# Kernel optimization log

Measured on AMD Instinct MI355X. Metric: run time of the kernel, lower is better.

## Reference

```python
import jax, jax.numpy as jnp
import numpy as np

N = 50000        # nodes
E = 800000       # edges (before self-loops)
F_IN = 128       # input node features
HID = 64         # GAT hidden per head
HEADS1 = 4
NUM_GRAPHS = 64
NEG_SLOPE = 0.2  # PyG GATConv default leaky_relu slope


def setup_inputs() -> dict:
    key = jax.random.key(0)
    ks = jax.random.split(key, 12)
    x = jax.random.normal(ks[0], (N, F_IN), dtype=jnp.float32)
    edge_index = jax.random.randint(ks[1], (2, E), 0, N, dtype=jnp.int32)
    batch = jnp.sort(jax.random.randint(ks[2], (N,), 0, NUM_GRAPHS, dtype=jnp.int32))
    s = 1.0 / np.sqrt(F_IN)
    W1 = jax.random.uniform(ks[3], (F_IN, HEADS1 * HID), jnp.float32, -s, s)
    att_src1 = jax.random.uniform(ks[4], (HEADS1, HID), jnp.float32, -s, s)
    att_dst1 = jax.random.uniform(ks[5], (HEADS1, HID), jnp.float32, -s, s)
    b1 = jnp.zeros((HEADS1 * HID,), jnp.float32)
    s2 = 1.0 / np.sqrt(HEADS1 * HID)
    W2 = jax.random.uniform(ks[6], (HEADS1 * HID, HID), jnp.float32, -s2, s2)
    att_src2 = jax.random.uniform(ks[7], (1, HID), jnp.float32, -s2, s2)
    att_dst2 = jax.random.uniform(ks[8], (1, HID), jnp.float32, -s2, s2)
    b2 = jnp.zeros((HID,), jnp.float32)
    return {"x": x, "edge_index": edge_index, "batch": batch,
            "W1": W1, "att_src1": att_src1, "att_dst1": att_dst1, "b1": b1,
            "W2": W2, "att_src2": att_src2, "att_dst2": att_dst2, "b2": b2}


def gat_conv(x, src, dst, W, a_src, a_dst, bias, heads, out_dim):
    # PyG GATConv: h = x @ W (no lin bias); per-node attention logits;
    # e_ij = leaky_relu(alpha_src[j] + alpha_dst[i]); softmax over dst groups;
    # out_i = sum_j alpha_ij * h_j; concat heads; + bias.
    n = x.shape[0]
    h = (x @ W).reshape(n, heads, out_dim)                 # [N,H,C]
    alpha_src = jnp.einsum('nhc,hc->nh', h, a_src)         # [N,H]
    alpha_dst = jnp.einsum('nhc,hc->nh', h, a_dst)         # [N,H]
    e = jax.nn.leaky_relu(alpha_src[src] + alpha_dst[dst], NEG_SLOPE)  # [E,H]
    m = jax.ops.segment_max(e, dst, num_segments=n)        # segment softmax (stable)
    e = jnp.exp(e - m[dst])
    denom = jax.ops.segment_sum(e, dst, num_segments=n)
    alpha = e / denom[dst]                                 # [E,H]
    msg = h[src] * alpha[:, :, None]                       # [E,H,C]
    agg = jax.ops.segment_sum(msg, dst, num_segments=n)    # [N,H,C]
    return agg.reshape(n, heads * out_dim) + bias


def reference(x, edge_index, batch, W1, att_src1, att_dst1, b1, W2, att_src2, att_dst2, b2):
    # add self loops (PyG GATConv default add_self_loops=True)
    loops = jnp.arange(N, dtype=edge_index.dtype)
    src = jnp.concatenate([edge_index[0], loops])
    dst = jnp.concatenate([edge_index[1], loops])
    h = jax.nn.relu(gat_conv(x, src, dst, W1, att_src1, att_dst1, b1, HEADS1, HID))
    h = gat_conv(h, src, dst, W2, att_src2, att_dst2, b2, 1, HID)
    # global mean pool over graphs
    sums = jax.ops.segment_sum(h, batch, num_segments=NUM_GRAPHS)
    cnt = jax.ops.segment_sum(jnp.ones((N,), h.dtype), batch, num_segments=NUM_GRAPHS)
    return sums / jnp.maximum(cnt, 1.0)[:, None]
```

## Files before the change

kernel.cpp:

```cpp
#include <hip/hip_runtime.h>
#include <math.h>


typedef unsigned short ushort_t;
typedef __bf16 bf16x8 __attribute__((ext_vector_type(8)));
typedef float  f32x4  __attribute__((ext_vector_type(4)));

__device__ inline float bf2f(ushort_t u) { return __uint_as_float((unsigned)u << 16); }
__device__ inline ushort_t f2bf(float x) {
  unsigned b = __float_as_uint(x);
  return (ushort_t)((b + 0x7fff + ((b >> 16) & 1)) >> 16);
}
__device__ inline float leaky(float v) { return (v > 0.f) ? v : 0.2f * v; }

__device__ inline f32x4 mfma16(bf16x8 a, bf16x8 b, f32x4 c) {
  return __builtin_amdgcn_mfma_f32_16x16x32_bf16(a, b, c, 0, 0, 0);
}

__global__ void k_zero_i32(int* __restrict__ p, int n) {
  int i = blockIdx.x * blockDim.x + threadIdx.x;
  if (i < n) p[i] = 0;
}

__global__ void k_hist(const int* __restrict__ edst, int E, int N, int* __restrict__ deg) {
  int stride = gridDim.x * blockDim.x;
  int EE = E + N;
  for (int i = blockIdx.x * blockDim.x + threadIdx.x; i < EE; i += stride) {
    int d = (i < E) ? edst[i] : (i - E);
    atomicAdd(&deg[d], 1);
  }
}

__global__ void k_gbounds(const int* __restrict__ batch, int N, int G,
                          int* __restrict__ gstart) {
  int stride = gridDim.x * blockDim.x;
  for (int i = blockIdx.x * blockDim.x + threadIdx.x; i < N; i += stride) {
    int b = batch[i];
    int bp = (i == 0) ? -1 : batch[i - 1];
    for (int g = bp + 1; g <= b; ++g) gstart[g] = i;
    if (i == N - 1)
      for (int g = b + 1; g <= G; ++g) gstart[g] = N;
  }
}

__global__ void k_scan_bsum(const int* __restrict__ deg, int n, int* __restrict__ bsum) {
  __shared__ int ws[16];
  int tid = threadIdx.x, lane = tid & 63, wv = tid >> 6;
  int i = blockIdx.x * 1024 + tid;
  int v = (i < n) ? deg[i] : 0;
  #pragma unroll
  for (int off = 1; off < 64; off <<= 1) v += __shfl_xor(v, off);
  if (lane == 0) ws[wv] = v;
  __syncthreads();
  if (tid < 16) {
    int s = ws[tid];
    #pragma unroll
    for (int off = 1; off < 16; off <<= 1) s += __shfl_xor(s, off);
    if (tid == 0) bsum[blockIdx.x] = s;
  }
}

__global__ void k_scan_bbase(const int* __restrict__ bsum, int nb,
                             int* __restrict__ bbase, int* __restrict__ offsets, int n) {
  int lane = threadIdx.x & 63;
  int v = (lane < nb) ? bsum[lane] : 0;
  int x = v;
  #pragma unroll
  for (int off = 1; off < 64; off <<= 1) {
    int t = __shfl_up(x, off);
    if (lane >= off) x += t;
  }
  if (lane < nb) bbase[lane] = x - v;
  if (lane == nb - 1) offsets[n] = x;
}

__global__ void k_scan_final(const int* __restrict__ deg, int n,
                             const int* __restrict__ bbase,
                             int* __restrict__ offsets, int* __restrict__ cursor) {
  __shared__ int wsum[16];
  int tid = threadIdx.x, lane = tid & 63, wv = tid >> 6;
  int i = blockIdx.x * 1024 + tid;
  int v = (i < n) ? deg[i] : 0;
  int x = v;
  #pragma unroll
  for (int off = 1; off < 64; off <<= 1) {
    int t = __shfl_up(x, off);
    if (lane >= off) x += t;
  }
  if (lane == 63) wsum[wv] = x;
  __syncthreads();
  if (wv == 0 && lane < 16) {
    int s = wsum[lane];
    #pragma unroll
    for (int off = 1; off < 16; off <<= 1) {
      int t = __shfl_up(s, off);
      if (lane >= off) s += t;
    }
    wsum[lane] = s;
  }
  __syncthreads();
  int wbase = (wv == 0) ? 0 : wsum[wv - 1];
  int incl = bbase[blockIdx.x] + wbase + x;
  if (i < n) { int o = incl - v; offsets[i] = o; cursor[i] = o; }
}

__global__ void k_scatter(const int* __restrict__ esrc, const int* __restrict__ edst,
                          int E, int N, int* __restrict__ cursor,
                          int* __restrict__ ssrc, int* __restrict__ sdst) {
  int stride = gridDim.x * blockDim.x;
  int EE = E + N;
  for (int i = blockIdx.x * blockDim.x + threadIdx.x; i < EE; i += stride) {
    int d, s;
    if (i < E) { d = edst[i]; s = esrc[i]; }
    else       { d = i - E;   s = i - E;   }
    int pos = atomicAdd(&cursor[d], 1);
    ssrc[pos] = s;
    sdst[pos] = d;
  }
}


__global__ void k_packA_f32(const float* __restrict__ A, ushort_t* __restrict__ ah,
                            ushort_t* __restrict__ al, int M, int K, int MF) {
  int KT = K >> 5;
  int total = MF * KT * 64;
  int t = blockIdx.x * blockDim.x + threadIdx.x;
  if (t >= total) return;
  int l = t & 63, fa = t >> 6;
  int mt = fa / KT, kt = fa - mt * KT;
  int row = mt * 16 + (l & 15);
  int k0 = kt * 32 + (l >> 4) * 8;
  float v[8];
  if (row < M) {
    float4 v0 = *(const float4*)(A + (size_t)row * K + k0);
    float4 v1 = *(const float4*)(A + (size_t)row * K + k0 + 4);
    v[0] = v0.x; v[1] = v0.y; v[2] = v0.z; v[3] = v0.w;
    v[4] = v1.x; v[5] = v1.y; v[6] = v1.z; v[7] = v1.w;
  } else {
    #pragma unroll
    for (int j = 0; j < 8; ++j) v[j] = 0.f;
  }
  ushort_t h[8], lo[8];
  #pragma unroll
  for (int j = 0; j < 8; ++j) {
    h[j] = f2bf(v[j]);
    lo[j] = f2bf(v[j] - bf2f(h[j]));
  }
  size_t o = (size_t)t * 8;
  *(ushort4*)(ah + o)     = make_ushort4(h[0], h[1], h[2], h[3]);
  *(ushort4*)(ah + o + 4) = make_ushort4(h[4], h[5], h[6], h[7]);
  *(ushort4*)(al + o)     = make_ushort4(lo[0], lo[1], lo[2], lo[3]);
  *(ushort4*)(al + o + 4) = make_ushort4(lo[4], lo[5], lo[6], lo[7]);
}

__global__ void k_packB_f32(const float* __restrict__ B, ushort_t* __restrict__ bh,
                            ushort_t* __restrict__ bl, int K, int Nn) {
  int KT = K >> 5;
  int total = (Nn >> 4) * KT * 64;
  int t = blockIdx.x * blockDim.x + threadIdx.x;
  if (t >= total) return;
  int l = t & 63, fb = t >> 6;
  int nt = fb / KT, kt = fb - nt * KT;
  int col = nt * 16 + (l & 15);
  int k0 = kt * 32 + (l >> 4) * 8;
  ushort_t h[8], lo[8];
  #pragma unroll
  for (int j = 0; j < 8; ++j) {
    float v = B[(size_t)(k0 + j) * Nn + col];
    h[j] = f2bf(v);
    lo[j] = f2bf(v - bf2f(h[j]));
  }
  size_t o = (size_t)t * 8;
  *(ushort4*)(bh + o)     = make_ushort4(h[0], h[1], h[2], h[3]);
  *(ushort4*)(bh + o + 4) = make_ushort4(h[4], h[5], h[6], h[7]);
  *(ushort4*)(bl + o)     = make_ushort4(lo[0], lo[1], lo[2], lo[3]);
  *(ushort4*)(bl + o + 4) = make_ushort4(lo[4], lo[5], lo[6], lo[7]);
}

template<int KT, int TERMS, int WM>
__global__ __launch_bounds__(256)
void k_gemm_att(const ushort_t* __restrict__ Ah, const ushort_t* __restrict__ Al,
                const ushort_t* __restrict__ Bh, const ushort_t* __restrict__ Bl,
                const float* __restrict__ a_srcW, const float* __restrict__ a_dstW,
                ushort_t* __restrict__ hb, float* __restrict__ as_,
                float* __restrict__ ad_, int M, int Nn, int H) {
  constexpr int WN = 4 / WM;
  const int tid = threadIdx.x;
  const int w = tid >> 6, lane = tid & 63;
  const int wm = w & (WM - 1), wn = w / WM;
  const int m0w = blockIdx.x * (WM * 32) + wm * 32;
  const int n0  = blockIdx.y * (WN * 64) + wn * 64;
  const int head = n0 >> 6;
  const int mt0 = m0w >> 4, nt0 = n0 >> 4;

  const ushort_t* pAh[2];
  const ushort_t* pAl[2];
  const ushort_t* pBh[4];
  const ushort_t* pBl[4];
  #pragma unroll
  for (int mi = 0; mi < 2; ++mi) {
    size_t fa = (size_t)(mt0 + mi) * KT;
    pAh[mi] = Ah + fa * 512 + (size_t)lane * 8;
    if constexpr (TERMS == 3) pAl[mi] = Al + fa * 512 + (size_t)lane * 8;
  }
  #pragma unroll
  for (int ni = 0; ni < 4; ++ni) {
    size_t fb = (size_t)(nt0 + ni) * KT;
    pBh[ni] = Bh + fb * 512 + (size_t)lane * 8;
    pBl[ni] = Bl + fb * 512 + (size_t)lane * 8;
  }

  f32x4 acc[2][4];
  #pragma unroll
  for (int mi = 0; mi < 2; ++mi)
    #pragma unroll
    for (int ni = 0; ni < 4; ++ni)
      acc[mi][ni] = (f32x4){0.f, 0.f, 0.f, 0.f};

  for (int kt = 0; kt < KT; ++kt) {
    const size_t ko = (size_t)kt * 512;
    bf16x8 ahf[2], alf[2], bhf[4], blf[4];
    #pragma unroll
    for (int mi = 0; mi < 2; ++mi) {
      ahf[mi] = *(const bf16x8*)(pAh[mi] + ko);
      if constexpr (TERMS == 3) alf[mi] = *(const bf16x8*)(pAl[mi] + ko);
    }
    #pragma unroll
    for (int ni = 0; ni < 4; ++ni) {
      bhf[ni] = *(const bf16x8*)(pBh[ni] + ko);
      blf[ni] = *(const bf16x8*)(pBl[ni] + ko);
    }
    #pragma unroll
    for (int mi = 0; mi < 2; ++mi)
      #pragma unroll
      for (int ni = 0; ni < 4; ++ni) {
        if constexpr (TERMS == 3)
          acc[mi][ni] = mfma16(alf[mi], bhf[ni], acc[mi][ni]);
        acc[mi][ni] = mfma16(ahf[mi], blf[ni], acc[mi][ni]);
        acc[mi][ni] = mfma16(ahf[mi], bhf[ni], acc[mi][ni]);
      }
  }

  const int c16 = lane & 15, q = lane >> 4;
  float sv[4], dv[4];
  #pragma unroll
  for (int ni = 0; ni < 4; ++ni) {
    sv[ni] = a_srcW[head * 64 + ni * 16 + c16];
    dv[ni] = a_dstW[head * 64 + ni * 16 + c16];
  }
  #pragma unroll
  for (int mi = 0; mi < 2; ++mi) {
    #pragma unroll
    for (int r = 0; r < 4; ++r) {
      int gr = m0w + mi * 16 + q * 4 + r;
      float ps = acc[mi][0][r] * sv[0] + acc[mi][1][r] * sv[1] +
                 acc[mi][2][r] * sv[2] + acc[mi][3][r] * sv[3];
      float pd = acc[mi][0][r] * dv[0] + acc[mi][1][r] * dv[1] +
                 acc[mi][2][r] * dv[2] + acc[mi][3][r] * dv[3];
      #pragma unroll
      for (int off = 1; off < 16; off <<= 1) {
        ps += __shfl_xor(ps, off);
        pd += __shfl_xor(pd, off);
      }
      if (gr < M) {
        #pragma unroll
        for (int ni = 0; ni < 4; ++ni)
          hb[(size_t)gr * Nn + n0 + ni * 16 + c16] = f2bf(acc[mi][ni][r]);
        if (c16 == 0) { as_[gr * H + head] = ps; ad_[gr * H + head] = pd; }
      }
    }
  }
}

__global__ void k_edgew1(const int* __restrict__ ssrc, const int* __restrict__ sdst,
                         const float* __restrict__ as1, const float* __restrict__ ad1,
                         float* __restrict__ w1, int EE) {
  int t = blockIdx.x * blockDim.x + threadIdx.x;
  if (t >= EE * 4) return;
  int e = t >> 2, h = t & 3;
  int s = ssrc[e], d = sdst[e];
  w1[t] = __expf(leaky(as1[s * 4 + h] + ad1[d * 4 + h]));
}

__global__ void k_edgew2(const int* __restrict__ ssrc, const int* __restrict__ sdst,
                         const float* __restrict__ as2, const float* __restrict__ ad2,
                         float* __restrict__ w2, int EE) {
  int e = blockIdx.x * blockDim.x + threadIdx.x;
  if (e >= EE) return;
  w2[e] = __expf(leaky(as2[ssrc[e]] + ad2[sdst[e]]));
}

__global__ void k_agg1(const ushort_t* __restrict__ h1b, const float* __restrict__ w1,
                       const int* __restrict__ offs, const int* __restrict__ ssrc,
                       const float* __restrict__ b1, ushort_t* __restrict__ a2h, int N) {
  int gt = blockIdx.x * blockDim.x + threadIdx.x;
  int wid = gt >> 6, lane = gt & 63;
  if (wid >= N) return;
  int head = lane >> 4, sub = lane & 15, coff = sub << 2;
  int start = offs[wid], end = offs[wid + 1];

  float denom = 0.f;
  float4 acc = make_float4(0.f, 0.f, 0.f, 0.f);
  int e = start;
  for (; e + 8 <= end; e += 8) {
    int s0 = ssrc[e], s1 = ssrc[e + 1], s2 = ssrc[e + 2], s3 = ssrc[e + 3];
    int s4 = ssrc[e + 4], s5 = ssrc[e + 5], s6 = ssrc[e + 6], s7 = ssrc[e + 7];
    float wa = w1[(e + 0) * 4 + head], wb = w1[(e + 1) * 4 + head];
    float wc = w1[(e + 2) * 4 + head], wd = w1[(e + 3) * 4 + head];
    float we = w1[(e + 4) * 4 + head], wf = w1[(e + 5) * 4 + head];
    float wg = w1[(e + 6) * 4 + head], wh = w1[(e + 7) * 4 + head];
    ushort4 g0 = *(const ushort4*)(h1b + (size_t)s0 * 256 + head * 64 + coff);
    ushort4 g1 = *(const ushort4*)(h1b + (size_t)s1 * 256 + head * 64 + coff);
    ushort4 g2 = *(const ushort4*)(h1b + (size_t)s2 * 256 + head * 64 + coff);
    ushort4 g3 = *(const ushort4*)(h1b + (size_t)s3 * 256 + head * 64 + coff);
    ushort4 g4 = *(const ushort4*)(h1b + (size_t)s4 * 256 + head * 64 + coff);
    ushort4 g5 = *(const ushort4*)(h1b + (size_t)s5 * 256 + head * 64 + coff);
    ushort4 g6 = *(const ushort4*)(h1b + (size_t)s6 * 256 + head * 64 + coff);
    ushort4 g7 = *(const ushort4*)(h1b + (size_t)s7 * 256 + head * 64 + coff);
    denom += ((wa + wb) + (wc + wd)) + ((we + wf) + (wg + wh));
    acc.x += wa * bf2f(g0.x) + wb * bf2f(g1.x) + wc * bf2f(g2.x) + wd * bf2f(g3.x)
           + we * bf2f(g4.x) + wf * bf2f(g5.x) + wg * bf2f(g6.x) + wh * bf2f(g7.x);
    acc.y += wa * bf2f(g0.y) + wb * bf2f(g1.y) + wc * bf2f(g2.y) + wd * bf2f(g3.y)
           + we * bf2f(g4.y) + wf * bf2f(g5.y) + wg * bf2f(g6.y) + wh * bf2f(g7.y);
    acc.z += wa * bf2f(g0.z) + wb * bf2f(g1.z) + wc * bf2f(g2.z) + wd * bf2f(g3.z)
           + we * bf2f(g4.z) + wf * bf2f(g5.z) + wg * bf2f(g6.z) + wh * bf2f(g7.z);
    acc.w += wa * bf2f(g0.w) + wb * bf2f(g1.w) + wc * bf2f(g2.w) + wd * bf2f(g3.w)
           + we * bf2f(g4.w) + wf * bf2f(g5.w) + wg * bf2f(g6.w) + wh * bf2f(g7.w);
  }
  for (; e + 4 <= end; e += 4) {
    int s0 = ssrc[e], s1 = ssrc[e + 1], s2 = ssrc[e + 2], s3 = ssrc[e + 3];
    float wa = w1[(e + 0) * 4 + head], wb = w1[(e + 1) * 4 + head];
    float wc = w1[(e + 2) * 4 + head], wd = w1[(e + 3) * 4 + head];
    ushort4 g0 = *(const ushort4*)(h1b + (size_t)s0 * 256 + head * 64 + coff);
    ushort4 g1 = *(const ushort4*)(h1b + (size_t)s1 * 256 + head * 64 + coff);
    ushort4 g2 = *(const ushort4*)(h1b + (size_t)s2 * 256 + head * 64 + coff);
    ushort4 g3 = *(const ushort4*)(h1b + (size_t)s3 * 256 + head * 64 + coff);
    denom += (wa + wb) + (wc + wd);
    acc.x += wa * bf2f(g0.x) + wb * bf2f(g1.x) + wc * bf2f(g2.x) + wd * bf2f(g3.x);
    acc.y += wa * bf2f(g0.y) + wb * bf2f(g1.y) + wc * bf2f(g2.y) + wd * bf2f(g3.y);
    acc.z += wa * bf2f(g0.z) + wb * bf2f(g1.z) + wc * bf2f(g2.z) + wd * bf2f(g3.z);
    acc.w += wa * bf2f(g0.w) + wb * bf2f(g1.w) + wc * bf2f(g2.w) + wd * bf2f(g3.w);
  }
  for (; e < end; ++e) {
    int s = ssrc[e];
    float w = w1[e * 4 + head];
    ushort4 g = *(const ushort4*)(h1b + (size_t)s * 256 + head * 64 + coff);
    denom += w;
    acc.x += w * bf2f(g.x); acc.y += w * bf2f(g.y);
    acc.z += w * bf2f(g.z); acc.w += w * bf2f(g.w);
  }
  float inv = 1.f / denom;
  float4 bv = *(const float4*)(b1 + head * 64 + coff);
  int c0 = head * 64 + coff;
  int fa = (wid >> 4) * 8 + (c0 >> 5);
  int fl = (wid & 15) | (((c0 >> 3) & 3) << 4);
  size_t addr = ((size_t)fa * 64 + fl) * 8 + (c0 & 7);
  ushort4 o;
  o.x = f2bf(fmaxf(acc.x * inv + bv.x, 0.f));
  o.y = f2bf(fmaxf(acc.y * inv + bv.y, 0.f));
  o.z = f2bf(fmaxf(acc.z * inv + bv.z, 0.f));
  o.w = f2bf(fmaxf(acc.w * inv + bv.w, 0.f));
  *(ushort4*)(a2h + addr) = o;
}

__global__ void k_agg2(const ushort_t* __restrict__ h2b, const float* __restrict__ w2,
                       const int* __restrict__ offs, const int* __restrict__ ssrc,
                       const float* __restrict__ b2, float* __restrict__ hfin, int N) {
  int gt = blockIdx.x * blockDim.x + threadIdx.x;
  int wid = gt >> 6, lane = gt & 63;
  if (wid >= N) return;
  int half = lane >> 5, li = lane & 31;
  int start = offs[wid], end = offs[wid + 1];

  float dn = 0.f, acc0 = 0.f, acc1 = 0.f;
  int e = start;
  for (; e + 8 <= end; e += 8) {
    int e0 = e + half, e1 = e + 2 + half, e2 = e + 4 + half, e3 = e + 6 + half;
    int s0 = ssrc[e0], s1 = ssrc[e1], s2 = ssrc[e2], s3 = ssrc[e3];
    float wa = w2[e0], wb = w2[e1], wc = w2[e2], wd = w2[e3];
    unsigned g0 = *(const unsigned*)(h2b + (size_t)s0 * 64 + li * 2);
    unsigned g1 = *(const unsigned*)(h2b + (size_t)s1 * 64 + li * 2);
    unsigned g2 = *(const unsigned*)(h2b + (size_t)s2 * 64 + li * 2);
    unsigned g3 = *(const unsigned*)(h2b + (size_t)s3 * 64 + li * 2);
    dn += (wa + wb) + (wc + wd);
    acc0 += wa * __uint_as_float(g0 << 16) + wb * __uint_as_float(g1 << 16)
          + wc * __uint_as_float(g2 << 16) + wd * __uint_as_float(g3 << 16);
    acc1 += wa * __uint_as_float(g0 & 0xffff0000u) + wb * __uint_as_float(g1 & 0xffff0000u)
          + wc * __uint_as_float(g2 & 0xffff0000u) + wd * __uint_as_float(g3 & 0xffff0000u);
  }
  for (; e + 2 <= end; e += 2) {
    int e0 = e + half;
    int s0 = ssrc[e0];
    float wa = w2[e0];
    unsigned g0 = *(const unsigned*)(h2b + (size_t)s0 * 64 + li * 2);
    dn += wa;
    acc0 += wa * __uint_as_float(g0 << 16);
    acc1 += wa * __uint_as_float(g0 & 0xffff0000u);
  }
  if (e < end && half == 0) {
    int s0 = ssrc[e];
    float wa = w2[e];
    unsigned g0 = *(const unsigned*)(h2b + (size_t)s0 * 64 + li * 2);
    dn += wa;
    acc0 += wa * __uint_as_float(g0 << 16);
    acc1 += wa * __uint_as_float(g0 & 0xffff0000u);
  }
  acc0 += __shfl_xor(acc0, 32);
  acc1 += __shfl_xor(acc1, 32);
  dn   += __shfl_xor(dn, 32);
  if (half == 0) {
    float inv = 1.f / dn;
    float2 bv = *(const float2*)(b2 + li * 2);
    float2 o;
    o.x = acc0 * inv + bv.x;
    o.y = acc1 * inv + bv.y;
    *(float2*)(hfin + (size_t)wid * 64 + li * 2) = o;
  }
}

__global__ void k_pool(const float* __restrict__ hfin, const int* __restrict__ gstart,
                       float* __restrict__ out) {
  int g = blockIdx.x;
  int c = threadIdx.x & 63, r = threadIdx.x >> 6;
  int start = gstart[g], cnt = gstart[g + 1] - start;
  float acc = 0.f;
  for (int i = r; i < cnt; i += 4)
    acc += hfin[(size_t)(start + i) * 64 + c];
  __shared__ float red[256];
  red[threadIdx.x] = acc;
  __syncthreads();
  if (r == 0)
    out[g * 64 + c] = (red[c] + red[64 + c] + red[128 + c] + red[192 + c]) /
                      fmaxf((float)cnt, 1.f);
}

extern "C" void kernel_launch(void* const* d_in, const int* in_sizes, int n_in,
                              void* d_out, int out_size, void* d_ws, size_t ws_size,
                              hipStream_t stream) {
  const float* x        = (const float*)d_in[0];
  const int*   ei       = (const int*)d_in[1];
  const int*   batch    = (const int*)d_in[2];
  const float* W1       = (const float*)d_in[3];
  const float* att_src1 = (const float*)d_in[4];
  const float* att_dst1 = (const float*)d_in[5];
  const float* b1       = (const float*)d_in[6];
  const float* W2       = (const float*)d_in[7];
  const float* att_src2 = (const float*)d_in[8];
  const float* att_dst2 = (const float*)d_in[9];
  const float* b2       = (const float*)d_in[10];
  float* out = (float*)d_out;

  const int N = in_sizes[0] / 128;
  const int E = in_sizes[1] / 2;
  const int EE = E + N;
  const int* esrc = ei;
  const int* edst = ei + E;

  const int GB2 = (N + 127) / 128;
  const int GB1 = GB2 * 2;
  const int MF  = GB2 * 8;
  const int NB  = (N + 1023) / 1024;

  char* p = (char*)d_ws;
  auto alloc = [&](size_t bytes) -> void* {
    void* r = (void*)p;
    p += (bytes + 255) & ~(size_t)255;
    return r;
  };
  ushort_t* A1h  = (ushort_t*)alloc((size_t)MF * 4 * 64 * 16);
  ushort_t* A1l  = (ushort_t*)alloc((size_t)MF * 4 * 64 * 16);
  ushort_t* A2h  = (ushort_t*)alloc((size_t)MF * 8 * 64 * 16);
  ushort_t* B1h  = (ushort_t*)alloc((size_t)16 * 4 * 64 * 16);
  ushort_t* B1l  = (ushort_t*)alloc((size_t)16 * 4 * 64 * 16);
  ushort_t* B2h  = (ushort_t*)alloc((size_t)4 * 8 * 64 * 16);
  ushort_t* B2l  = (ushort_t*)alloc((size_t)4 * 8 * 64 * 16);
  ushort_t* h1b  = (ushort_t*)alloc((size_t)N * 256 * 2);
  ushort_t* h2b  = (ushort_t*)alloc((size_t)N * 64 * 2);
  float*    hfin = (float*)alloc((size_t)N * 64 * 4);
  float*    as1  = (float*)alloc((size_t)N * 4 * 4);
  float*    ad1  = (float*)alloc((size_t)N * 4 * 4);
  float*    as2  = (float*)alloc((size_t)N * 4);
  float*    ad2  = (float*)alloc((size_t)N * 4);
  float*    w1   = (float*)alloc((size_t)EE * 4 * 4);
  float*    w2   = (float*)alloc((size_t)EE * 4);
  int* deg     = (int*)alloc((size_t)N * 4);
  int* offsets = (int*)alloc((size_t)(N + 1) * 4);
  int* cursor  = (int*)alloc((size_t)N * 4);
  int* ssrc    = (int*)alloc((size_t)EE * 4);
  int* sdst    = (int*)alloc((size_t)EE * 4);
  int* bsum    = (int*)alloc(64 * 4);
  int* bbase   = (int*)alloc(64 * 4);
  int* gstart  = (int*)alloc(65 * 4);

  k_zero_i32<<<(N + 255) / 256, 256, 0, stream>>>(deg, N);
  k_hist<<<1024, 256, 0, stream>>>(edst, E, N, deg);
  k_gbounds<<<256, 256, 0, stream>>>(batch, N, 64, gstart);
  k_scan_bsum<<<NB, 1024, 0, stream>>>(deg, N, bsum);
  k_scan_bbase<<<1, 64, 0, stream>>>(bsum, NB, bbase, offsets, N);
  k_scan_final<<<NB, 1024, 0, stream>>>(deg, N, bbase, offsets, cursor);
  k_scatter<<<1024, 256, 0, stream>>>(esrc, edst, E, N, cursor, ssrc, sdst);

  k_packB_f32<<<16, 256, 0, stream>>>(W1, B1h, B1l, 128, 256);
  k_packB_f32<<<8, 256, 0, stream>>>(W2, B2h, B2l, 256, 64);
  k_packA_f32<<<MF * 4 * 64 / 256, 256, 0, stream>>>(x, A1h, A1l, N, 128, MF);

  k_gemm_att<4, 3, 2><<<dim3(GB1, 2), 256, 0, stream>>>(
      A1h, A1l, B1h, B1l, att_src1, att_dst1, h1b, as1, ad1, N, 256, 4);
  k_edgew1<<<(EE * 4 + 255) / 256, 256, 0, stream>>>(ssrc, sdst, as1, ad1, w1, EE);
  int wave_blocks = (N * 64 + 255) / 256;
  k_agg1<<<wave_blocks, 256, 0, stream>>>(h1b, w1, offsets, ssrc, b1, A2h, N);

  k_gemm_att<8, 2, 4><<<dim3(GB2, 1), 256, 0, stream>>>(
      A2h, nullptr, B2h, B2l, att_src2, att_dst2, h2b, as2, ad2, N, 64, 1);
  k_edgew2<<<(EE + 255) / 256, 256, 0, stream>>>(ssrc, sdst, as2, ad2, w2, EE);
  k_agg2<<<wave_blocks, 256, 0, stream>>>(h2b, w2, offsets, ssrc, b2, hfin, N);

  k_pool<<<64, 256, 0, stream>>>(hfin, gstart, out);
}
```

Baseline: 305.6 us.

## Fuse x packing into GEMM, merge setup kernels, interleave edge src/dst arrays

The layer-1 GEMM now reads fp32 x directly and splits it into bf16 hi/lo in registers, which removes the separate A-packing kernel and its intermediate buffers. The degree zeroing is folded into the graph-bounds kernel, and the two B-packing launches are merged into one. Sorted edge src/dst are stored as interleaved int2 so the edge-weight kernels do a single load per edge. The cost is that the aggregation kernels now read 8-byte int2 records when they only need src, which doubles their index traffic, and the GEMM repeats the conversion work in each block that shares the same rows.

```diff
diff --git a/kernel.cpp b/kernel.cpp
--- a/kernel.cpp
+++ b/kernel.cpp
@@ -15,11 +15,6 @@
 
 __device__ inline f32x4 mfma16(bf16x8 a, bf16x8 b, f32x4 c) {
   return __builtin_amdgcn_mfma_f32_16x16x32_bf16(a, b, c, 0, 0, 0);
-}
-
-__global__ void k_zero_i32(int* __restrict__ p, int n) {
-  int i = blockIdx.x * blockDim.x + threadIdx.x;
-  if (i < n) p[i] = 0;
 }
 
 __global__ void k_hist(const int* __restrict__ edst, int E, int N, int* __restrict__ deg) {
@@ -31,10 +26,11 @@
   }
 }
 
-__global__ void k_gbounds(const int* __restrict__ batch, int N, int G,
-                          int* __restrict__ gstart) {
+__global__ void k_gbounds_zero(const int* __restrict__ batch, int N, int G,
+                               int* __restrict__ gstart, int* __restrict__ deg) {
   int stride = gridDim.x * blockDim.x;
   for (int i = blockIdx.x * blockDim.x + threadIdx.x; i < N; i += stride) {
+    deg[i] = 0;
     int b = batch[i];
     int bp = (i == 0) ? -1 : batch[i - 1];
     for (int g = bp + 1; g <= b; ++g) gstart[g] = i;
@@ -106,7 +102,7 @@
 
 __global__ void k_scatter(const int* __restrict__ esrc, const int* __restrict__ edst,
                           int E, int N, int* __restrict__ cursor,
-                          int* __restrict__ ssrc, int* __restrict__ sdst) {
+                          int2* __restrict__ sed) {
   int stride = gridDim.x * blockDim.x;
   int EE = E + N;
   for (int i = blockIdx.x * blockDim.x + threadIdx.x; i < EE; i += stride) {
@@ -114,51 +110,13 @@
     if (i < E) { d = edst[i]; s = esrc[i]; }
     else       { d = i - E;   s = i - E;   }
     int pos = atomicAdd(&cursor[d], 1);
-    ssrc[pos] = s;
-    sdst[pos] = d;
-  }
-}
-
-
-__global__ void k_packA_f32(const float* __restrict__ A, ushort_t* __restrict__ ah,
-                            ushort_t* __restrict__ al, int M, int K, int MF) {
+    sed[pos] = make_int2(s, d);
+  }
+}
+
+__device__ inline void packB_one(const float* __restrict__ B, ushort_t* __restrict__ bh,
+                                 ushort_t* __restrict__ bl, int K, int Nn, int t) {
   int KT = K >> 5;
-  int total = MF * KT * 64;
-  int t = blockIdx.x * blockDim.x + threadIdx.x;
-  if (t >= total) return;
-  int l = t & 63, fa = t >> 6;
-  int mt = fa / KT, kt = fa - mt * KT;
-  int row = mt * 16 + (l & 15);
-  int k0 = kt * 32 + (l >> 4) * 8;
-  float v[8];
-  if (row < M) {
-    float4 v0 = *(const float4*)(A + (size_t)row * K + k0);
-    float4 v1 = *(const float4*)(A + (size_t)row * K + k0 + 4);
-    v[0] = v0.x; v[1] = v0.y; v[2] = v0.z; v[3] = v0.w;
-    v[4] = v1.x; v[5] = v1.y; v[6] = v1.z; v[7] = v1.w;
-  } else {
-    #pragma unroll
-    for (int j = 0; j < 8; ++j) v[j] = 0.f;
-  }
-  ushort_t h[8], lo[8];
-  #pragma unroll
-  for (int j = 0; j < 8; ++j) {
-    h[j] = f2bf(v[j]);
-    lo[j] = f2bf(v[j] - bf2f(h[j]));
-  }
-  size_t o = (size_t)t * 8;
-  *(ushort4*)(ah + o)     = make_ushort4(h[0], h[1], h[2], h[3]);
-  *(ushort4*)(ah + o + 4) = make_ushort4(h[4], h[5], h[6], h[7]);
-  *(ushort4*)(al + o)     = make_ushort4(lo[0], lo[1], lo[2], lo[3]);
-  *(ushort4*)(al + o + 4) = make_ushort4(lo[4], lo[5], lo[6], lo[7]);
-}
-
-__global__ void k_packB_f32(const float* __restrict__ B, ushort_t* __restrict__ bh,
-                            ushort_t* __restrict__ bl, int K, int Nn) {
-  int KT = K >> 5;
-  int total = (Nn >> 4) * KT * 64;
-  int t = blockIdx.x * blockDim.x + threadIdx.x;
-  if (t >= total) return;
   int l = t & 63, fb = t >> 6;
   int nt = fb / KT, kt = fb - nt * KT;
   int col = nt * 16 + (l & 15);
@@ -177,32 +135,44 @@
   *(ushort4*)(bl + o + 4) = make_ushort4(lo[4], lo[5], lo[6], lo[7]);
 }
 
+__global__ void k_packB_all(const float* __restrict__ W1, const float* __restrict__ W2,
+                            ushort_t* __restrict__ B1h, ushort_t* __restrict__ B1l,
+                            ushort_t* __restrict__ B2h, ushort_t* __restrict__ B2l) {
+  int t = blockIdx.x * blockDim.x + threadIdx.x;
+  if (t < 4096) packB_one(W1, B1h, B1l, 128, 256, t);
+  else if (t < 6144) packB_one(W2, B2h, B2l, 256, 64, t - 4096);
+}
+
 template<int KT, int TERMS, int WM>
 __global__ __launch_bounds__(256)
-void k_gemm_att(const ushort_t* __restrict__ Ah, const ushort_t* __restrict__ Al,
+void k_gemm_att(const float* __restrict__ Af32, const ushort_t* __restrict__ Ah,
                 const ushort_t* __restrict__ Bh, const ushort_t* __restrict__ Bl,
                 const float* __restrict__ a_srcW, const float* __restrict__ a_dstW,
                 ushort_t* __restrict__ hb, float* __restrict__ as_,
                 float* __restrict__ ad_, int M, int Nn, int H) {
-  constexpr int WN = 4 / WM;
   const int tid = threadIdx.x;
   const int w = tid >> 6, lane = tid & 63;
   const int wm = w & (WM - 1), wn = w / WM;
   const int m0w = blockIdx.x * (WM * 32) + wm * 32;
-  const int n0  = blockIdx.y * (WN * 64) + wn * 64;
+  const int n0  = blockIdx.y * ((4 / WM) * 64) + wn * 64;
   const int head = n0 >> 6;
   const int mt0 = m0w >> 4, nt0 = n0 >> 4;
 
+  const float* pX[2];
+  int rowmi[2];
   const ushort_t* pAh[2];
-  const ushort_t* pAl[2];
+  #pragma unroll
+  for (int mi = 0; mi < 2; ++mi) {
+    if constexpr (TERMS == 3) {
+      rowmi[mi] = (mt0 + mi) * 16 + (lane & 15);
+      pX[mi] = Af32 + (size_t)rowmi[mi] * (KT * 32) + ((lane >> 4) << 3);
+    } else {
+      size_t fa = (size_t)(mt0 + mi) * KT;
+      pAh[mi] = Ah + fa * 512 + (size_t)lane * 8;
+    }
+  }
   const ushort_t* pBh[4];
   const ushort_t* pBl[4];
-  #pragma unroll
-  for (int mi = 0; mi < 2; ++mi) {
-    size_t fa = (size_t)(mt0 + mi) * KT;
-    pAh[mi] = Ah + fa * 512 + (size_t)lane * 8;
-    if constexpr (TERMS == 3) pAl[mi] = Al + fa * 512 + (size_t)lane * 8;
-  }
   #pragma unroll
   for (int ni = 0; ni < 4; ++ni) {
     size_t fb = (size_t)(nt0 + ni) * KT;
@@ -222,8 +192,25 @@
     bf16x8 ahf[2], alf[2], bhf[4], blf[4];
     #pragma unroll
     for (int mi = 0; mi < 2; ++mi) {
-      ahf[mi] = *(const bf16x8*)(pAh[mi] + ko);
-      if constexpr (TERMS == 3) alf[mi] = *(const bf16x8*)(pAl[mi] + ko);
+      if constexpr (TERMS == 3) {
+        float v[8] = {0.f, 0.f, 0.f, 0.f, 0.f, 0.f, 0.f, 0.f};
+        if (rowmi[mi] < M) {
+          float4 a = *(const float4*)(pX[mi] + kt * 32);
+          float4 b = *(const float4*)(pX[mi] + kt * 32 + 4);
+          v[0] = a.x; v[1] = a.y; v[2] = a.z; v[3] = a.w;
+          v[4] = b.x; v[5] = b.y; v[6] = b.z; v[7] = b.w;
+        }
+        union { ushort_t u[8]; bf16x8 f; } uh, ul;
+        #pragma unroll
+        for (int j = 0; j < 8; ++j) {
+          uh.u[j] = f2bf(v[j]);
+          ul.u[j] = f2bf(v[j] - bf2f(uh.u[j]));
+        }
+        ahf[mi] = uh.f;
+        alf[mi] = ul.f;
+      } else {
+        ahf[mi] = *(const bf16x8*)(pAh[mi] + ko);
+      }
     }
     #pragma unroll
     for (int ni = 0; ni < 4; ++ni) {
@@ -272,26 +259,25 @@
   }
 }
 
-__global__ void k_edgew1(const int* __restrict__ ssrc, const int* __restrict__ sdst,
-                         const float* __restrict__ as1, const float* __restrict__ ad1,
-                         float* __restrict__ w1, int EE) {
+__global__ void k_edgew1(const int2* __restrict__ sed, const float* __restrict__ as1,
+                         const float* __restrict__ ad1, float* __restrict__ w1, int EE) {
   int t = blockIdx.x * blockDim.x + threadIdx.x;
   if (t >= EE * 4) return;
   int e = t >> 2, h = t & 3;
-  int s = ssrc[e], d = sdst[e];
-  w1[t] = __expf(leaky(as1[s * 4 + h] + ad1[d * 4 + h]));
-}
-
-__global__ void k_edgew2(const int* __restrict__ ssrc, const int* __restrict__ sdst,
-                         const float* __restrict__ as2, const float* __restrict__ ad2,
-                         float* __restrict__ w2, int EE) {
+  int2 p = sed[e];
+  w1[t] = __expf(leaky(as1[p.x * 4 + h] + ad1[p.y * 4 + h]));
+}
+
+__global__ void k_edgew2(const int2* __restrict__ sed, const float* __restrict__ as2,
+                         const float* __restrict__ ad2, float* __restrict__ w2, int EE) {
   int e = blockIdx.x * blockDim.x + threadIdx.x;
   if (e >= EE) return;
-  w2[e] = __expf(leaky(as2[ssrc[e]] + ad2[sdst[e]]));
+  int2 p = sed[e];
+  w2[e] = __expf(leaky(as2[p.x] + ad2[p.y]));
 }
 
 __global__ void k_agg1(const ushort_t* __restrict__ h1b, const float* __restrict__ w1,
-                       const int* __restrict__ offs, const int* __restrict__ ssrc,
+                       const int* __restrict__ offs, const int2* __restrict__ sed,
                        const float* __restrict__ b1, ushort_t* __restrict__ a2h, int N) {
   int gt = blockIdx.x * blockDim.x + threadIdx.x;
   int wid = gt >> 6, lane = gt & 63;
@@ -303,8 +289,8 @@
   float4 acc = make_float4(0.f, 0.f, 0.f, 0.f);
   int e = start;
   for (; e + 8 <= end; e += 8) {
-    int s0 = ssrc[e], s1 = ssrc[e + 1], s2 = ssrc[e + 2], s3 = ssrc[e + 3];
-    int s4 = ssrc[e + 4], s5 = ssrc[e + 5], s6 = ssrc[e + 6], s7 = ssrc[e + 7];
+    int s0 = sed[e].x, s1 = sed[e + 1].x, s2 = sed[e + 2].x, s3 = sed[e + 3].x;
+    int s4 = sed[e + 4].x, s5 = sed[e + 5].x, s6 = sed[e + 6].x, s7 = sed[e + 7].x;
     float wa = w1[(e + 0) * 4 + head], wb = w1[(e + 1) * 4 + head];
     float wc = w1[(e + 2) * 4 + head], wd = w1[(e + 3) * 4 + head];
     float we = w1[(e + 4) * 4 + head], wf = w1[(e + 5) * 4 + head];
@@ -328,7 +314,7 @@
            + we * bf2f(g4.w) + wf * bf2f(g5.w) + wg * bf2f(g6.w) + wh * bf2f(g7.w);
   }
   for (; e + 4 <= end; e += 4) {
-    int s0 = ssrc[e], s1 = ssrc[e + 1], s2 = ssrc[e + 2], s3 = ssrc[e + 3];
+    int s0 = sed[e].x, s1 = sed[e + 1].x, s2 = sed[e + 2].x, s3 = sed[e + 3].x;
     float wa = w1[(e + 0) * 4 + head], wb = w1[(e + 1) * 4 + head];
     float wc = w1[(e + 2) * 4 + head], wd = w1[(e + 3) * 4 + head];
     ushort4 g0 = *(const ushort4*)(h1b + (size_t)s0 * 256 + head * 64 + coff);
@@ -342,7 +328,7 @@
     acc.w += wa * bf2f(g0.w) + wb * bf2f(g1.w) + wc * bf2f(g2.w) + wd * bf2f(g3.w);
   }
   for (; e < end; ++e) {
-    int s = ssrc[e];
+    int s = sed[e].x;
     float w = w1[e * 4 + head];
     ushort4 g = *(const ushort4*)(h1b + (size_t)s * 256 + head * 64 + coff);
     denom += w;
@@ -364,7 +350,7 @@
 }
 
 __global__ void k_agg2(const ushort_t* __restrict__ h2b, const float* __restrict__ w2,
-                       const int* __restrict__ offs, const int* __restrict__ ssrc,
+                       const int* __restrict__ offs, const int2* __restrict__ sed,
                        const float* __restrict__ b2, float* __restrict__ hfin, int N) {
   int gt = blockIdx.x * blockDim.x + threadIdx.x;
   int wid = gt >> 6, lane = gt & 63;
@@ -376,7 +362,7 @@
   int e = start;
   for (; e + 8 <= end; e += 8) {
     int e0 = e + half, e1 = e + 2 + half, e2 = e + 4 + half, e3 = e + 6 + half;
-    int s0 = ssrc[e0], s1 = ssrc[e1], s2 = ssrc[e2], s3 = ssrc[e3];
+    int s0 = sed[e0].x, s1 = sed[e1].x, s2 = sed[e2].x, s3 = sed[e3].x;
     float wa = w2[e0], wb = w2[e1], wc = w2[e2], wd = w2[e3];
     unsigned g0 = *(const unsigned*)(h2b + (size_t)s0 * 64 + li * 2);
     unsigned g1 = *(const unsigned*)(h2b + (size_t)s1 * 64 + li * 2);
@@ -390,7 +376,7 @@
   }
   for (; e + 2 <= end; e += 2) {
     int e0 = e + half;
-    int s0 = ssrc[e0];
+    int s0 = sed[e0].x;
     float wa = w2[e0];
     unsigned g0 = *(const unsigned*)(h2b + (size_t)s0 * 64 + li * 2);
     dn += wa;
@@ -398,7 +384,7 @@
     acc1 += wa * __uint_as_float(g0 & 0xffff0000u);
   }
   if (e < end && half == 0) {
-    int s0 = ssrc[e];
+    int s0 = sed[e].x;
     float wa = w2[e];
     unsigned g0 = *(const unsigned*)(h2b + (size_t)s0 * 64 + li * 2);
     dn += wa;
@@ -467,8 +453,6 @@
     p += (bytes + 255) & ~(size_t)255;
     return r;
   };
-  ushort_t* A1h  = (ushort_t*)alloc((size_t)MF * 4 * 64 * 16);
-  ushort_t* A1l  = (ushort_t*)alloc((size_t)MF * 4 * 64 * 16);
   ushort_t* A2h  = (ushort_t*)alloc((size_t)MF * 8 * 64 * 16);
   ushort_t* B1h  = (ushort_t*)alloc((size_t)16 * 4 * 64 * 16);
   ushort_t* B1l  = (ushort_t*)alloc((size_t)16 * 4 * 64 * 16);
@@ -483,37 +467,33 @@
   float*    ad2  = (float*)alloc((size_t)N * 4);
   float*    w1   = (float*)alloc((size_t)EE * 4 * 4);
   float*    w2   = (float*)alloc((size_t)EE * 4);
-  int* deg     = (int*)alloc((size_t)N * 4);
-  int* offsets = (int*)alloc((size_t)(N + 1) * 4);
-  int* cursor  = (int*)alloc((size_t)N * 4);
-  int* ssrc    = (int*)alloc((size_t)EE * 4);
-  int* sdst    = (int*)alloc((size_t)EE * 4);
-  int* bsum    = (int*)alloc(64 * 4);
-  int* bbase   = (int*)alloc(64 * 4);
-  int* gstart  = (int*)alloc(65 * 4);
-
-  k_zero_i32<<<(N + 255) / 256, 256, 0, stream>>>(deg, N);
+  int*  deg     = (int*)alloc((size_t)N * 4);
+  int*  offsets = (int*)alloc((size_t)(N + 1) * 4);
+  int*  cursor  = (int*)alloc((size_t)N * 4);
+  int2* sed     = (int2*)alloc((size_t)EE * 8);
+  int*  bsum    = (int*)alloc(64 * 4);
+  int*  bbase   = (int*)alloc(64 * 4);
+  int*  gstart  = (int*)alloc(65 * 4);
+
+  k_gbounds_zero<<<256, 256, 0, stream>>>(batch, N, 64, gstart, deg);
   k_hist<<<1024, 256, 0, stream>>>(edst, E, N, deg);
-  k_gbounds<<<256, 256, 0, stream>>>(batch, N, 64, gstart);
   k_scan_bsum<<<NB, 1024, 0, stream>>>(deg, N, bsum);
   k_scan_bbase<<<1, 64, 0, stream>>>(bsum, NB, bbase, offsets, N);
   k_scan_final<<<NB, 1024, 0, stream>>>(deg, N, bbase, offsets, cursor);
-  k_scatter<<<1024, 256, 0, stream>>>(esrc, edst, E, N, cursor, ssrc, sdst);
-
-  k_packB_f32<<<16, 256, 0, stream>>>(W1, B1h, B1l, 128, 256);
-  k_packB_f32<<<8, 256, 0, stream>>>(W2, B2h, B2l, 256, 64);
-  k_packA_f32<<<MF * 4 * 64 / 256, 256, 0, stream>>>(x, A1h, A1l, N, 128, MF);
+  k_scatter<<<1024, 256, 0, stream>>>(esrc, edst, E, N, cursor, sed);
+
+  k_packB_all<<<24, 256, 0, stream>>>(W1, W2, B1h, B1l, B2h, B2l);
 
   k_gemm_att<4, 3, 2><<<dim3(GB1, 2), 256, 0, stream>>>(
-      A1h, A1l, B1h, B1l, att_src1, att_dst1, h1b, as1, ad1, N, 256, 4);
-  k_edgew1<<<(EE * 4 + 255) / 256, 256, 0, stream>>>(ssrc, sdst, as1, ad1, w1, EE);
+      x, nullptr, B1h, B1l, att_src1, att_dst1, h1b, as1, ad1, N, 256, 4);
+  k_edgew1<<<(EE * 4 + 255) / 256, 256, 0, stream>>>(sed, as1, ad1, w1, EE);
   int wave_blocks = (N * 64 + 255) / 256;
-  k_agg1<<<wave_blocks, 256, 0, stream>>>(h1b, w1, offsets, ssrc, b1, A2h, N);
+  k_agg1<<<wave_blocks, 256, 0, stream>>>(h1b, w1, offsets, sed, b1, A2h, N);
 
   k_gemm_att<8, 2, 4><<<dim3(GB2, 1), 256, 0, stream>>>(
-      A2h, nullptr, B2h, B2l, att_src2, att_dst2, h2b, as2, ad2, N, 64, 1);
-  k_edgew2<<<(EE + 255) / 256, 256, 0, stream>>>(ssrc, sdst, as2, ad2, w2, EE);
-  k_agg2<<<wave_blocks, 256, 0, stream>>>(h2b, w2, offsets, ssrc, b2, hfin, N);
+      nullptr, A2h, B2h, B2l, att_src2, att_dst2, h2b, as2, ad2, N, 64, 1);
+  k_edgew2<<<(EE + 255) / 256, 256, 0, stream>>>(sed, as2, ad2, w2, EE);
+  k_agg2<<<wave_blocks, 256, 0, stream>>>(h2b, w2, offsets, sed, b2, hfin, N);
 
   k_pool<<<64, 256, 0, stream>>>(hfin, gstart, out);
 }
```

Result: no change. 308.9 us (+1.1%).
